# Kernel tuning notes

Measured on AMD Instinct MI355X. Metric: run time of the kernel, lower is better.

Reference implementation:

```python
import jax, jax.numpy as jnp
import numpy as np

B, D, K, C, A = 131072, 300, 32, 384, 18  # batch, emb dim, num_negs, codebook size, attr dims


def setup_inputs() -> dict:
    key = jax.random.key(0)
    ks = jax.random.split(key, 12)
    x = jax.random.normal(ks[0], (B, D), dtype=jnp.float32)
    # codebook of all possible attribute one-hot combinations (binary rows)
    codebook = (jax.random.uniform(ks[1], (C, A)) < 0.5).astype(jnp.float32)
    tgt = jax.random.randint(ks[2], (B,), 0, C)
    y = codebook[tgt]                                   # true labels are codebook rows
    ob = (jax.random.uniform(ks[3], (B, A)) > 0.1).astype(jnp.float32)  # observed-attr mask
    neg_idx = jax.random.randint(ks[4], (B, K), 0, C)   # negative sample indices
    s = 0.05
    W1 = jax.random.normal(ks[5], (D, 64), dtype=jnp.float32) * s
    b1 = jnp.zeros((64,), jnp.float32)
    W2 = jax.random.normal(ks[6], (64, 32), dtype=jnp.float32) * s
    b2 = jnp.zeros((32,), jnp.float32)
    W3 = jax.random.normal(ks[7], (32, A), dtype=jnp.float32) * s
    b3 = jnp.zeros((A,), jnp.float32)
    return dict(x=x, y=y, ob=ob, codebook=codebook, W1=W1, b1=b1, W2=W2, b2=b2,
                W3=W3, b3=b3, neg_idx=neg_idx)


def reference(x, y, ob, codebook, W1, b1, W2, b2, W3, b3, neg_idx):
    # MLP: Linear->Sigmoid->Linear->Sigmoid->Linear
    h = jax.nn.sigmoid(x @ W1 + b1)
    h = jax.nn.sigmoid(h @ W2 + b2)
    W_user = h @ W3 + b3                                # [B, A]
    W_compact = W_user * ob                             # [B, A]
    # rows kept by the original index_select: nonzero row-sum -> mask instead
    mask = (jnp.sum(W_compact, axis=1) != 0).astype(W_compact.dtype)  # [B]
    neg = codebook[neg_idx]                             # [B, K, A] gather
    # neg log term: sum over negatives and attr dims of log sigmoid(-(neg * w))
    neg_log = jax.nn.log_sigmoid(-neg * W_compact[:, None, :]).sum(axis=(1, 2))  # [B]
    pos_log = jax.nn.log_sigmoid(W_compact * y).sum(axis=1)                      # [B]
    cnt = jnp.maximum(jnp.sum(mask), 1.0)
    loss = -jnp.sum(mask * (pos_log + neg_log)) / cnt
    return W_user, loss
```

## Files before the change

kernel.cpp:

```cpp
#include <hip/hip_runtime.h>

typedef short bf16x8 __attribute__((ext_vector_type(8)));
typedef unsigned short u16;
typedef u16 u16x4 __attribute__((ext_vector_type(4)));
typedef float f32x4 __attribute__((ext_vector_type(4)));

constexpr int TPB  = 256;
constexpr int RPB  = 64;
constexpr int DIM  = 300;
constexpr int KPAD = 320;
constexpr int NKT  = 10;
constexpr int H1N  = 64;
constexpr int H2N  = 32;
constexpr int NA   = 18;
constexpr int NK   = 32;
constexpr int NC   = 384;
constexpr float LOG_HALF = -0.6931471805599453f;

__device__ __forceinline__ float fast_sigmoid(float z) {
    return __builtin_amdgcn_rcpf(1.0f + __expf(-z));
}
__device__ __forceinline__ float lsig(float z) {
    return fminf(z, 0.0f) - __logf(1.0f + __expf(-fabsf(z)));
}
__device__ __forceinline__ u16 f2bf(float f) {
    unsigned u = __builtin_bit_cast(unsigned, f);
    return (u16)((u + 0x7FFFu + ((u >> 16) & 1u)) >> 16);
}
__device__ __forceinline__ unsigned spread8(unsigned v) {
    v = (v | (v << 12)) & 0x000F000Fu;
    v = (v | (v << 6))  & 0x03030303u;
    v = (v | (v << 3))  & 0x11111111u;
    return v;
}

__global__ __launch_bounds__(384)
void prep_k(const float* __restrict__ W1, const float* __restrict__ W2,
            const float* __restrict__ W3, const float* __restrict__ cbf,
            u16* __restrict__ w1t, u16* __restrict__ w2t, u16* __restrict__ w3t,
            unsigned* __restrict__ cbw)
{
    const int c = blockIdx.x;
    const int t = threadIdx.x;
    if (c < 64) {
        if (t < KPAD)
            w1t[c * KPAD + t] = f2bf((t < DIM) ? W1[t * H1N + c] : 0.0f);
    } else if (c == 64) {
        if (t < NC) {
            unsigned bits = 0u;
            #pragma unroll
            for (int a = 0; a < NA; ++a)
                bits |= (cbf[t * NA + a] != 0.0f) ? (1u << a) : 0u;
            cbw[t] = bits;
        }
    } else if (c == 65) {
        for (int e = t; e < H2N * H1N; e += 384) {
            const int n = e >> 6, k = e & 63;
            w2t[e] = f2bf(W2[k * H2N + n]);
        }
    } else {
        for (int e = t; e < H2N * H2N; e += 384) {
            const int n = e >> 5, k = e & 31;
            w3t[e] = f2bf((n < NA) ? W3[k * NA + n] : 0.0f);
        }
    }
}

__global__ __launch_bounds__(TPB, 4)
void fused_mf2(const float* __restrict__ x, const float* __restrict__ y,
               const float* __restrict__ ob, const float* __restrict__ b1,
               const float* __restrict__ b2, const float* __restrict__ b3,
               const int* __restrict__ neg_idx,
               const u16* __restrict__ w1t, const u16* __restrict__ w2t,
               const u16* __restrict__ w3t, const unsigned* __restrict__ cbw,
               float* __restrict__ out_wu, float2* __restrict__ blk_part)
{
    __shared__ __align__(16) unsigned char smem[40960];
    u16*      xs      = (u16*)smem;
    u16*      h1s     = (u16*)smem;
    u16*      h2s     = (u16*)(smem + 8192);
    float*    wus     = (float*)(smem + 12288);
    unsigned* cb_bits = (unsigned*)(smem + 17408);
    float*    wsum    = (float*)(smem + 18944);
    int*      wcnt    = (int*)(smem + 18960);

    const int tid  = threadIdx.x;
    const int lane = tid & 63;
    const int wv   = tid >> 6;
    const int l15  = lane & 15;
    const int kg   = (lane >> 4) * 8;
    const long brow = (long)blockIdx.x * RPB;
    const float* xg = x + brow * DIM;

    float4 v[19];
    #pragma unroll
    for (int ch = 0; ch < 19; ++ch) {
        const int f = ch * TPB + tid;
        v[ch] = (ch < 18 || f < 4800) ? *(const float4*)(xg + (long)f * 4)
                                      : make_float4(0.f, 0.f, 0.f, 0.f);
    }
    __builtin_amdgcn_sched_barrier(0);
    #pragma unroll
    for (int ch = 0; ch < 19; ++ch) {
        const int f = ch * TPB + tid;
        if (ch < 18 || f < 4800) {
            const int row = f / 75, k = (f - row * 75) * 4;
            const int kk = k ^ ((row & 7) << 3);
            u16x4 pk = { f2bf(v[ch].x), f2bf(v[ch].y), f2bf(v[ch].z), f2bf(v[ch].w) };
            *(u16x4*)(xs + row * KPAD + kk) = pk;
        }
    }
    #pragma unroll
    for (int uu = 0; uu < 5; ++uu) {
        const int e = uu * TPB + tid;
        const int row = e / 20, kp = e - row * 20;
        xs[row * KPAD + ((DIM + kp) ^ ((row & 7) << 3))] = 0;
    }

    const int colB = wv * 16 + l15;
    bf16x8 bfr[NKT];
    #pragma unroll
    for (int kt = 0; kt < NKT; ++kt)
        bfr[kt] = *(const bf16x8*)(w1t + colB * KPAD + kt * 32 + kg);

    __syncthreads();

    f32x4 acc[4];
    #pragma unroll
    for (int rt = 0; rt < 4; ++rt) acc[rt] = (f32x4){0.f, 0.f, 0.f, 0.f};
    #pragma unroll
    for (int kt = 0; kt < NKT; ++kt) {
        bf16x8 afr[4];
        #pragma unroll
        for (int rt = 0; rt < 4; ++rt) {
            const int row = rt * 16 + l15;
            afr[rt] = *(const bf16x8*)(xs + ((row * KPAD + kt * 32 + kg) ^ ((row & 7) << 3)));
        }
        #pragma unroll
        for (int rt = 0; rt < 4; ++rt)
            acc[rt] = __builtin_amdgcn_mfma_f32_16x16x32_bf16(afr[rt], bfr[kt], acc[rt], 0, 0, 0);
    }
    __syncthreads();

    const float b1v = b1[colB];
    #pragma unroll
    for (int rt = 0; rt < 4; ++rt) {
        #pragma unroll
        for (int j = 0; j < 4; ++j) {
            const int row = rt * 16 + (lane >> 4) * 4 + j;
            h1s[(row * H1N + colB) ^ ((row & 7) << 3)] = f2bf(fast_sigmoid(acc[rt][j] + b1v));
        }
    }
    cb_bits[tid] = cbw[tid];
    if (tid < NC - TPB) cb_bits[tid + TPB] = cbw[tid + TPB];

    const int rloc = wv * 16 + (lane >> 2);
    const int p    = lane & 3;
    const long bds = brow + rloc;
    const int4* nbp = (const int4*)(neg_idx + bds * NK + p * 8);
    const int4 n0 = nbp[0], n1 = nbp[1];
    const float* obr = ob + bds * NA + p * 4;
    const float2 oA = *(const float2*)obr, oB = *(const float2*)(obr + 2);
    const float  oT = (p < 2) ? ob[bds * NA + 16 + p] : 0.f;
    const float* yr = y + bds * NA + p * 4;
    const float2 yA = *(const float2*)yr, yB = *(const float2*)(yr + 2);
    const float  yT = (p < 2) ? y[bds * NA + 16 + p] : 0.f;

    __syncthreads();

    const int rowA = wv * 16 + l15;
    bf16x8 a2[2];
    #pragma unroll
    for (int kt = 0; kt < 2; ++kt)
        a2[kt] = *(const bf16x8*)(h1s + ((rowA * H1N + kt * 32 + kg) ^ ((rowA & 7) << 3)));
    f32x4 acc2[2];
    #pragma unroll
    for (int ct = 0; ct < 2; ++ct) {
        const float bb = b2[ct * 16 + l15];
        acc2[ct] = (f32x4){bb, bb, bb, bb};
    }
    #pragma unroll
    for (int ct = 0; ct < 2; ++ct)
        #pragma unroll
        for (int kt = 0; kt < 2; ++kt) {
            const bf16x8 bfr2 = *(const bf16x8*)(w2t + (ct * 16 + l15) * H1N + kt * 32 + kg);
            acc2[ct] = __builtin_amdgcn_mfma_f32_16x16x32_bf16(a2[kt], bfr2, acc2[ct], 0, 0, 0);
        }
    #pragma unroll
    for (int ct = 0; ct < 2; ++ct) {
        #pragma unroll
        for (int j = 0; j < 4; ++j) {
            const int row = wv * 16 + (lane >> 4) * 4 + j;
            const int col = ct * 16 + l15;
            h2s[(row * H2N + col) ^ ((row & 3) << 3)] = f2bf(fast_sigmoid(acc2[ct][j]));
        }
    }

    const bf16x8 a3 = *(const bf16x8*)(h2s + ((rowA * H2N + kg) ^ ((rowA & 3) << 3)));
    f32x4 acc3[2];
    #pragma unroll
    for (int ct = 0; ct < 2; ++ct) {
        const int col = ct * 16 + l15;
        const float bb = (col < NA) ? b3[col] : 0.f;
        acc3[ct] = (f32x4){bb, bb, bb, bb};
    }
    #pragma unroll
    for (int ct = 0; ct < 2; ++ct) {
        const bf16x8 bfr3 = *(const bf16x8*)(w3t + (ct * 16 + l15) * H2N + kg);
        acc3[ct] = __builtin_amdgcn_mfma_f32_16x16x32_bf16(a3, bfr3, acc3[ct], 0, 0, 0);
    }
    #pragma unroll
    for (int j = 0; j < 4; ++j) {
        const int row = wv * 16 + (lane >> 4) * 4 + j;
        wus[row * 20 + l15] = acc3[0][j];
        if (l15 < 2) wus[row * 20 + 16 + l15] = acc3[1][j];
    }
    __builtin_amdgcn_sched_barrier(0);

    const float4 wA = *(const float4*)(wus + rloc * 20 + p * 4);
    const float  wT = (p < 2) ? wus[rloc * 20 + 16 + p] : 0.f;

    const float wcv[4] = {wA.x * oA.x, wA.y * oA.y, wA.z * oB.x, wA.w * oB.y};
    const float yvv[4] = {yA.x, yA.y, yB.x, yB.y};
    const float wcT = wT * oT;
    float ssum = wcv[0] + wcv[1] + wcv[2] + wcv[3] + wcT;
    ssum += __shfl_xor(ssum, 1);
    ssum += __shfl_xor(ssum, 2);
    const int mask = (ssum != 0.0f) ? 1 : 0;

    const int ids[8] = {n0.x, n0.y, n0.z, n0.w, n1.x, n1.y, n1.z, n1.w};
    unsigned c0 = 0u, c1 = 0u, c2 = 0u;
    #pragma unroll
    for (int kk = 0; kk < 8; ++kk) {
        const unsigned bits = cb_bits[ids[kk]];
        c0 += spread8(bits & 0xFFu);
        c1 += spread8((bits >> 8) & 0xFFu);
        const unsigned t = (bits >> 16) & 3u;
        c2 += (t | (t << 3)) & 0x11u;
    }
    unsigned e0 = c0 & 0x0F0F0F0Fu;
    unsigned e1 = (c0 >> 4) & 0x0F0F0F0Fu;
    unsigned e2 = c1 & 0x0F0F0F0Fu;
    unsigned e3 = (c1 >> 4) & 0x0F0F0F0Fu;
    unsigned e4 = (c2 & 15u) | (((c2 >> 4) & 15u) << 8);
    e0 += __shfl_xor((int)e0, 1); e0 += __shfl_xor((int)e0, 2);
    e1 += __shfl_xor((int)e1, 1); e1 += __shfl_xor((int)e1, 2);
    e2 += __shfl_xor((int)e2, 1); e2 += __shfl_xor((int)e2, 2);
    e3 += __shfl_xor((int)e3, 1); e3 += __shfl_xor((int)e3, 2);
    e4 += __shfl_xor((int)e4, 1); e4 += __shfl_xor((int)e4, 2);

    float rsum = 0.0f;
    #pragma unroll
    for (int i = 0; i < 4; ++i) {
        const unsigned regE = ((i & 1) == 0) ? ((p < 2) ? e0 : e2)
                                             : ((p < 2) ? e1 : e3);
        const int sh = (((p & 1) * 2) + (i >> 1)) * 8;
        const int cn = (int)((regE >> sh) & 0xFFu);
        const float w = wcv[i];
        const float pos = (yvv[i] != 0.0f) ? lsig(w) : LOG_HALF;
        rsum += pos + (float)cn * lsig(-w) + (float)(NK - cn) * LOG_HALF;
    }
    if (p < 2) {
        const int cn = (int)((e4 >> (p * 8)) & 0xFFu);
        const float pos = (yT != 0.0f) ? lsig(wcT) : LOG_HALF;
        rsum += pos + (float)cn * lsig(-wcT) + (float)(NK - cn) * LOG_HALF;
    }
    rsum += __shfl_xor(rsum, 1);
    rsum += __shfl_xor(rsum, 2);

    float vv = (p == 0 && mask) ? rsum : 0.0f;
    int   mm = (p == 0) ? mask : 0;
    #pragma unroll
    for (int off = 32; off > 0; off >>= 1) {
        vv += __shfl_down(vv, off);
        mm += __shfl_down(mm, off);
    }
    if (lane == 0) { wsum[wv] = vv; wcnt[wv] = mm; }
    __syncthreads();

    float* og = out_wu + brow * NA;
    #pragma unroll
    for (int g = tid; g < RPB * NA; g += TPB) {
        const int row = g / NA, col = g - row * NA;
        og[g] = wus[row * 20 + col];
    }
    if (tid == 0) {
        const float s = wsum[0] + wsum[1] + wsum[2] + wsum[3];
        const int   c = wcnt[0] + wcnt[1] + wcnt[2] + wcnt[3];
        blk_part[blockIdx.x] = make_float2(s, (float)c);
    }
}

__global__ void finalize_k(const float2* __restrict__ part, int nblk,
                           float* __restrict__ out_loss) {
    __shared__ float ss[4], sc[4];
    float s = 0.f, c = 0.f;
    for (int i = threadIdx.x; i < nblk; i += 256) {
        const float2 v = part[i];
        s += v.x; c += v.y;
    }
    #pragma unroll
    for (int off = 32; off > 0; off >>= 1) {
        s += __shfl_down(s, off);
        c += __shfl_down(c, off);
    }
    const int wv = threadIdx.x >> 6;
    if ((threadIdx.x & 63) == 0) { ss[wv] = s; sc[wv] = c; }
    __syncthreads();
    if (threadIdx.x == 0) {
        const float S = ss[0] + ss[1] + ss[2] + ss[3];
        const float C = sc[0] + sc[1] + sc[2] + sc[3];
        out_loss[0] = -S / fmaxf(C, 1.0f);
    }
}

extern "C" void kernel_launch(void* const* d_in, const int* in_sizes, int n_in,
                              void* d_out, int out_size, void* d_ws, size_t ws_size,
                              hipStream_t stream)
{
    const float* x   = (const float*)d_in[0];
    const float* y   = (const float*)d_in[1];
    const float* ob  = (const float*)d_in[2];
    const float* cb  = (const float*)d_in[3];
    const float* W1  = (const float*)d_in[4];
    const float* b1  = (const float*)d_in[5];
    const float* W2  = (const float*)d_in[6];
    const float* b2  = (const float*)d_in[7];
    const float* W3  = (const float*)d_in[8];
    const float* b3  = (const float*)d_in[9];
    const int*   neg = (const int*)d_in[10];

    const int B = in_sizes[0] / DIM;
    const int nblk = B / RPB;

    float*    out_wu = (float*)d_out;
    u16*      w1t  = (u16*)d_ws;
    u16*      w2t  = (u16*)((char*)d_ws + 40960);
    u16*      w3t  = (u16*)((char*)d_ws + 45056);
    unsigned* cbw  = (unsigned*)((char*)d_ws + 47104);
    float2*   part = (float2*)((char*)d_ws + 48640);

    prep_k<<<67, 384, 0, stream>>>(W1, W2, W3, cb, w1t, w2t, w3t, cbw);
    fused_mf2<<<nblk, TPB, 0, stream>>>(x, y, ob, b1, b2, b3,
                                        neg, w1t, w2t, w3t, cbw, out_wu, part);
    finalize_k<<<1, TPB, 0, stream>>>(part, nblk, out_wu + (long)B * NA);
}
```

Before: 51.81 us.

## Split first GEMM K into two halves to shrink LDS and overlap loads

The x tile is now staged in two K-halves of 160 columns through a smaller 168-stride LDS buffer instead of one 320-wide swizzled buffer. The global loads for the second half are issued before the MFMAs on the first half so they overlap, and the codebook bit loads are hoisted early. Launch bounds rise to 5 blocks per CU to use the freed LDS. The cost is extra barriers, an unswizzled layout that may cause LDS bank conflicts, and tighter register limits.

Result: slower. 56.25 us (+8.6%).

```diff
diff --git a/kernel.cpp b/kernel.cpp
--- a/kernel.cpp
+++ b/kernel.cpp
@@ -9,7 +9,8 @@
 constexpr int RPB  = 64;
 constexpr int DIM  = 300;
 constexpr int KPAD = 320;
-constexpr int NKT  = 10;
+constexpr int HK   = 160;
+constexpr int XST  = 168;
 constexpr int H1N  = 64;
 constexpr int H2N  = 32;
 constexpr int NA   = 18;
@@ -66,7 +67,7 @@
     }
 }
 
-__global__ __launch_bounds__(TPB, 4)
+__global__ __launch_bounds__(TPB, 5)
 void fused_mf2(const float* __restrict__ x, const float* __restrict__ y,
                const float* __restrict__ ob, const float* __restrict__ b1,
                const float* __restrict__ b2, const float* __restrict__ b3,
@@ -75,7 +76,7 @@
                const u16* __restrict__ w3t, const unsigned* __restrict__ cbw,
                float* __restrict__ out_wu, float2* __restrict__ blk_part)
 {
-    __shared__ __align__(16) unsigned char smem[40960];
+    __shared__ __align__(16) unsigned char smem[RPB * XST * 2];
     u16*      xs      = (u16*)smem;
     u16*      h1s     = (u16*)smem;
     u16*      h2s     = (u16*)(smem + 8192);
@@ -92,53 +93,86 @@
     const long brow = (long)blockIdx.x * RPB;
     const float* xg = x + brow * DIM;
 
-    float4 v[19];
-    #pragma unroll
-    for (int ch = 0; ch < 19; ++ch) {
+    float4 v0[10];
+    #pragma unroll
+    for (int ch = 0; ch < 10; ++ch) {
         const int f = ch * TPB + tid;
-        v[ch] = (ch < 18 || f < 4800) ? *(const float4*)(xg + (long)f * 4)
-                                      : make_float4(0.f, 0.f, 0.f, 0.f);
-    }
+        const int row = f / 40, k4 = f - row * 40;
+        v0[ch] = *(const float4*)(xg + (long)row * DIM + k4 * 4);
+    }
+    const int colB = wv * 16 + l15;
+    bf16x8 bfr0[5];
+    #pragma unroll
+    for (int k5 = 0; k5 < 5; ++k5)
+        bfr0[k5] = *(const bf16x8*)(w1t + colB * KPAD + k5 * 32 + kg);
+    const unsigned cbv0 = cbw[tid];
+    const unsigned cbv1 = (tid < NC - TPB) ? cbw[tid + TPB] : 0u;
+
     __builtin_amdgcn_sched_barrier(0);
     #pragma unroll
-    for (int ch = 0; ch < 19; ++ch) {
+    for (int ch = 0; ch < 10; ++ch) {
         const int f = ch * TPB + tid;
-        if (ch < 18 || f < 4800) {
-            const int row = f / 75, k = (f - row * 75) * 4;
-            const int kk = k ^ ((row & 7) << 3);
-            u16x4 pk = { f2bf(v[ch].x), f2bf(v[ch].y), f2bf(v[ch].z), f2bf(v[ch].w) };
-            *(u16x4*)(xs + row * KPAD + kk) = pk;
+        const int row = f / 40, k4 = f - row * 40;
+        u16x4 pk = { f2bf(v0[ch].x), f2bf(v0[ch].y), f2bf(v0[ch].z), f2bf(v0[ch].w) };
+        *(u16x4*)(xs + row * XST + k4 * 4) = pk;
+    }
+    __syncthreads();
+
+    float4 v1[9];
+    #pragma unroll
+    for (int ch = 0; ch < 9; ++ch) {
+        const int f = ch * TPB + tid;
+        if (ch < 8 || tid < 2240 - 8 * TPB) {
+            const int row = f / 35, c4 = f - row * 35;
+            v1[ch] = *(const float4*)(xg + (long)row * DIM + HK + c4 * 4);
+        }
+    }
+
+    f32x4 acc[4];
+    #pragma unroll
+    for (int rt = 0; rt < 4; ++rt) acc[rt] = (f32x4){0.f, 0.f, 0.f, 0.f};
+    #pragma unroll
+    for (int k5 = 0; k5 < 5; ++k5) {
+        bf16x8 afr[4];
+        #pragma unroll
+        for (int rt = 0; rt < 4; ++rt)
+            afr[rt] = *(const bf16x8*)(xs + (rt * 16 + l15) * XST + k5 * 32 + kg);
+        #pragma unroll
+        for (int rt = 0; rt < 4; ++rt)
+            acc[rt] = __builtin_amdgcn_mfma_f32_16x16x32_bf16(afr[rt], bfr0[k5], acc[rt], 0, 0, 0);
+    }
+    __syncthreads();
+
+    bf16x8 bfr1[5];
+    #pragma unroll
+    for (int k5 = 0; k5 < 5; ++k5)
+        bfr1[k5] = *(const bf16x8*)(w1t + colB * KPAD + (5 + k5) * 32 + kg);
+    #pragma unroll
+    for (int ch = 0; ch < 9; ++ch) {
+        const int f = ch * TPB + tid;
+        if (ch < 8 || tid < 2240 - 8 * TPB) {
+            const int row = f / 35, c4 = f - row * 35;
+            u16x4 pk = { f2bf(v1[ch].x), f2bf(v1[ch].y), f2bf(v1[ch].z), f2bf(v1[ch].w) };
+            *(u16x4*)(xs + row * XST + c4 * 4) = pk;
         }
     }
     #pragma unroll
     for (int uu = 0; uu < 5; ++uu) {
         const int e = uu * TPB + tid;
         const int row = e / 20, kp = e - row * 20;
-        xs[row * KPAD + ((DIM + kp) ^ ((row & 7) << 3))] = 0;
-    }
-
-    const int colB = wv * 16 + l15;
-    bf16x8 bfr[NKT];
-    #pragma unroll
-    for (int kt = 0; kt < NKT; ++kt)
-        bfr[kt] = *(const bf16x8*)(w1t + colB * KPAD + kt * 32 + kg);
-
-    __syncthreads();
-
-    f32x4 acc[4];
-    #pragma unroll
-    for (int rt = 0; rt < 4; ++rt) acc[rt] = (f32x4){0.f, 0.f, 0.f, 0.f};
-    #pragma unroll
-    for (int kt = 0; kt < NKT; ++kt) {
+        xs[row * XST + 140 + kp] = 0;
+    }
+    __syncthreads();
+
+    #pragma unroll
+    for (int k5 = 0; k5 < 5; ++k5) {
         bf16x8 afr[4];
         #pragma unroll
-        for (int rt = 0; rt < 4; ++rt) {
-            const int row = rt * 16 + l15;
-            afr[rt] = *(const bf16x8*)(xs + ((row * KPAD + kt * 32 + kg) ^ ((row & 7) << 3)));
-        }
-        #pragma unroll
         for (int rt = 0; rt < 4; ++rt)
-            acc[rt] = __builtin_amdgcn_mfma_f32_16x16x32_bf16(afr[rt], bfr[kt], acc[rt], 0, 0, 0);
+            afr[rt] = *(const bf16x8*)(xs + (rt * 16 + l15) * XST + k5 * 32 + kg);
+        #pragma unroll
+        for (int rt = 0; rt < 4; ++rt)
+            acc[rt] = __builtin_amdgcn_mfma_f32_16x16x32_bf16(afr[rt], bfr1[k5], acc[rt], 0, 0, 0);
     }
     __syncthreads();
 
@@ -151,8 +185,8 @@
             h1s[(row * H1N + colB) ^ ((row & 7) << 3)] = f2bf(fast_sigmoid(acc[rt][j] + b1v));
         }
     }
-    cb_bits[tid] = cbw[tid];
-    if (tid < NC - TPB) cb_bits[tid + TPB] = cbw[tid + TPB];
+    cb_bits[tid] = cbv0;
+    if (tid < NC - TPB) cb_bits[tid + TPB] = cbv1;
 
     const int rloc = wv * 16 + (lane >> 2);
     const int p    = lane & 3;
```

## Fuse final loss reduction into main kernel via atomics and hoist weight loads

Applied to the files above, without the earlier changes.

Removes the separate finalize kernel launch by having each block atomically add its partial sum and count to global accumulators, with the last-arriving block computing the final loss. It also hoists the W1 fragment and codebook-bit global loads above the x conversion, so their latency overlaps the x loads. The ob/y/neg_idx loads now sit before the first barrier, ahead of the GEMM. This trades one kernel launch for 2048 double-precision atomics and a last-block pattern, and the higher register pressure from hoisting may affect occupancy.

Result: slower. 121.8 us (+135.0%).

```diff
diff --git a/kernel.cpp b/kernel.cpp
--- a/kernel.cpp
+++ b/kernel.cpp
@@ -38,7 +38,8 @@
 void prep_k(const float* __restrict__ W1, const float* __restrict__ W2,
             const float* __restrict__ W3, const float* __restrict__ cbf,
             u16* __restrict__ w1t, u16* __restrict__ w2t, u16* __restrict__ w3t,
-            unsigned* __restrict__ cbw)
+            unsigned* __restrict__ cbw, double* __restrict__ ls,
+            unsigned* __restrict__ cnts)
 {
     const int c = blockIdx.x;
     const int t = threadIdx.x;
@@ -53,6 +54,7 @@
                 bits |= (cbf[t * NA + a] != 0.0f) ? (1u << a) : 0u;
             cbw[t] = bits;
         }
+        if (t == 383) { *ls = 0.0; cnts[0] = 0u; cnts[1] = 0u; }
     } else if (c == 65) {
         for (int e = t; e < H2N * H1N; e += 384) {
             const int n = e >> 6, k = e & 63;
@@ -73,7 +75,8 @@
                const int* __restrict__ neg_idx,
                const u16* __restrict__ w1t, const u16* __restrict__ w2t,
                const u16* __restrict__ w3t, const unsigned* __restrict__ cbw,
-               float* __restrict__ out_wu, float2* __restrict__ blk_part)
+               float* __restrict__ out_wu, double* __restrict__ ls,
+               unsigned* __restrict__ cnts, float* __restrict__ out_loss)
 {
     __shared__ __align__(16) unsigned char smem[40960];
     u16*      xs      = (u16*)smem;
@@ -99,6 +102,14 @@
         v[ch] = (ch < 18 || f < 4800) ? *(const float4*)(xg + (long)f * 4)
                                       : make_float4(0.f, 0.f, 0.f, 0.f);
     }
+    const int colB = wv * 16 + l15;
+    bf16x8 bfr[NKT];
+    #pragma unroll
+    for (int kt = 0; kt < NKT; ++kt)
+        bfr[kt] = *(const bf16x8*)(w1t + colB * KPAD + kt * 32 + kg);
+    const unsigned cbv0 = cbw[tid];
+    const unsigned cbv1 = (tid < NC - TPB) ? cbw[tid + TPB] : 0u;
+
     __builtin_amdgcn_sched_barrier(0);
     #pragma unroll
     for (int ch = 0; ch < 19; ++ch) {
@@ -116,43 +127,6 @@
         const int row = e / 20, kp = e - row * 20;
         xs[row * KPAD + ((DIM + kp) ^ ((row & 7) << 3))] = 0;
     }
-
-    const int colB = wv * 16 + l15;
-    bf16x8 bfr[NKT];
-    #pragma unroll
-    for (int kt = 0; kt < NKT; ++kt)
-        bfr[kt] = *(const bf16x8*)(w1t + colB * KPAD + kt * 32 + kg);
-
-    __syncthreads();
-
-    f32x4 acc[4];
-    #pragma unroll
-    for (int rt = 0; rt < 4; ++rt) acc[rt] = (f32x4){0.f, 0.f, 0.f, 0.f};
-    #pragma unroll
-    for (int kt = 0; kt < NKT; ++kt) {
-        bf16x8 afr[4];
-        #pragma unroll
-        for (int rt = 0; rt < 4; ++rt) {
-            const int row = rt * 16 + l15;
-            afr[rt] = *(const bf16x8*)(xs + ((row * KPAD + kt * 32 + kg) ^ ((row & 7) << 3)));
-        }
-        #pragma unroll
-        for (int rt = 0; rt < 4; ++rt)
-            acc[rt] = __builtin_amdgcn_mfma_f32_16x16x32_bf16(afr[rt], bfr[kt], acc[rt], 0, 0, 0);
-    }
-    __syncthreads();
-
-    const float b1v = b1[colB];
-    #pragma unroll
-    for (int rt = 0; rt < 4; ++rt) {
-        #pragma unroll
-        for (int j = 0; j < 4; ++j) {
-            const int row = rt * 16 + (lane >> 4) * 4 + j;
-            h1s[(row * H1N + colB) ^ ((row & 7) << 3)] = f2bf(fast_sigmoid(acc[rt][j] + b1v));
-        }
-    }
-    cb_bits[tid] = cbw[tid];
-    if (tid < NC - TPB) cb_bits[tid + TPB] = cbw[tid + TPB];
 
     const int rloc = wv * 16 + (lane >> 2);
     const int p    = lane & 3;
@@ -168,6 +142,37 @@
 
     __syncthreads();
 
+    f32x4 acc[4];
+    #pragma unroll
+    for (int rt = 0; rt < 4; ++rt) acc[rt] = (f32x4){0.f, 0.f, 0.f, 0.f};
+    #pragma unroll
+    for (int kt = 0; kt < NKT; ++kt) {
+        bf16x8 afr[4];
+        #pragma unroll
+        for (int rt = 0; rt < 4; ++rt) {
+            const int row = rt * 16 + l15;
+            afr[rt] = *(const bf16x8*)(xs + ((row * KPAD + kt * 32 + kg) ^ ((row & 7) << 3)));
+        }
+        #pragma unroll
+        for (int rt = 0; rt < 4; ++rt)
+            acc[rt] = __builtin_amdgcn_mfma_f32_16x16x32_bf16(afr[rt], bfr[kt], acc[rt], 0, 0, 0);
+    }
+    __syncthreads();
+
+    const float b1v = b1[colB];
+    #pragma unroll
+    for (int rt = 0; rt < 4; ++rt) {
+        #pragma unroll
+        for (int j = 0; j < 4; ++j) {
+            const int row = rt * 16 + (lane >> 4) * 4 + j;
+            h1s[(row * H1N + colB) ^ ((row & 7) << 3)] = f2bf(fast_sigmoid(acc[rt][j] + b1v));
+        }
+    }
+    cb_bits[tid] = cbv0;
+    if (tid < NC - TPB) cb_bits[tid + TPB] = cbv1;
+
+    __syncthreads();
+
     const int rowA = wv * 16 + l15;
     bf16x8 a2[2];
     #pragma unroll
@@ -284,33 +289,20 @@
         const int row = g / NA, col = g - row * NA;
         og[g] = wus[row * 20 + col];
     }
+
     if (tid == 0) {
         const float s = wsum[0] + wsum[1] + wsum[2] + wsum[3];
         const int   c = wcnt[0] + wcnt[1] + wcnt[2] + wcnt[3];
-        blk_part[blockIdx.x] = make_float2(s, (float)c);
-    }
-}
-
-__global__ void finalize_k(const float2* __restrict__ part, int nblk,
-                           float* __restrict__ out_loss) {
-    __shared__ float ss[4], sc[4];
-    float s = 0.f, c = 0.f;
-    for (int i = threadIdx.x; i < nblk; i += 256) {
-        const float2 v = part[i];
-        s += v.x; c += v.y;
-    }
-    #pragma unroll
-    for (int off = 32; off > 0; off >>= 1) {
-        s += __shfl_down(s, off);
-        c += __shfl_down(c, off);
-    }
-    const int wv = threadIdx.x >> 6;
-    if ((threadIdx.x & 63) == 0) { ss[wv] = s; sc[wv] = c; }
-    __syncthreads();
-    if (threadIdx.x == 0) {
-        const float S = ss[0] + ss[1] + ss[2] + ss[3];
-        const float C = sc[0] + sc[1] + sc[2] + sc[3];
-        out_loss[0] = -S / fmaxf(C, 1.0f);
+        atomicAdd(ls, (double)s);
+        atomicAdd(&cnts[0], (unsigned)c);
+        __threadfence();
+        const unsigned prev = atomicAdd(&cnts[1], 1u);
+        if (prev == gridDim.x - 1) {
+            __threadfence();
+            const double S = atomicAdd(ls, 0.0);
+            const unsigned C = atomicAdd(&cnts[0], 0u);
+            out_loss[0] = (float)(-S / (double)(C > 0u ? C : 1u));
+        }
     }
 }
 
@@ -338,10 +330,11 @@
     u16*      w2t  = (u16*)((char*)d_ws + 40960);
     u16*      w3t  = (u16*)((char*)d_ws + 45056);
     unsigned* cbw  = (unsigned*)((char*)d_ws + 47104);
-    float2*   part = (float2*)((char*)d_ws + 48640);
-
-    prep_k<<<67, 384, 0, stream>>>(W1, W2, W3, cb, w1t, w2t, w3t, cbw);
+    double*   ls   = (double*)((char*)d_ws + 48640);
+    unsigned* cnts = (unsigned*)((char*)d_ws + 48648);
+
+    prep_k<<<67, 384, 0, stream>>>(W1, W2, W3, cb, w1t, w2t, w3t, cbw, ls, cnts);
     fused_mf2<<<nblk, TPB, 0, stream>>>(x, y, ob, b1, b2, b3,
-                                        neg, w1t, w2t, w3t, cbw, out_wu, part);
-    finalize_k<<<1, TPB, 0, stream>>>(part, nblk, out_wu + (long)B * NA);
-}
+                                        neg, w1t, w2t, w3t, cbw, out_wu,
+                                        ls, cnts, out_wu + (long)B * NA);
+}
```
